# Performance work log

Hardware: AMD Instinct MI355X
Metric: run time of the kernel (lower is better)

Reference implementation:

```python
import jax, jax.numpy as jnp
import numpy as np

D_MODEL = 1024
NUM_HEADS = 16
D_K = D_MODEL // NUM_HEADS
ROPE_BASE = 10000.0


def _rotate_half(x):
    # interleaved pairs: (x0, x1) -> (-x1, x0)
    x1 = x[..., ::2]
    x2 = x[..., 1::2]
    return jnp.stack((-x2, x1), axis=-1).reshape(x.shape)


def _rope(q, k):
    seq_len = q.shape[-2]
    freqs = ROPE_BASE ** (jnp.arange(0, D_K, 2, dtype=q.dtype) / D_K)  # [D_K/2]
    angles = jnp.arange(seq_len, dtype=q.dtype)[:, None] / freqs[None, :]  # [S, D_K/2]
    sin = jnp.repeat(jnp.sin(angles), 2, axis=-1)[None, None]  # [1,1,S,D_K]
    cos = jnp.repeat(jnp.cos(angles), 2, axis=-1)[None, None]
    return q * cos + _rotate_half(q) * sin, k * cos + _rotate_half(k) * sin


def setup_inputs() -> dict:
    key = jax.random.key(0)
    ks = jax.random.split(key, 9)
    B, S, D = 2, 2048, D_MODEL
    s = 1.0 / np.sqrt(D)
    inp = {
        "x": jax.random.normal(ks[0], (B, S, D), dtype=jnp.float32),
        "wq": jax.random.uniform(ks[1], (D, D), jnp.float32, -s, s),
        "bq": jax.random.uniform(ks[2], (D,), jnp.float32, -s, s),
        "wk": jax.random.uniform(ks[3], (D, D), jnp.float32, -s, s),
        "bk": jax.random.uniform(ks[4], (D,), jnp.float32, -s, s),
        "wv": jax.random.uniform(ks[5], (D, D), jnp.float32, -s, s),
        "bv": jax.random.uniform(ks[6], (D,), jnp.float32, -s, s),
        "wo": jax.random.uniform(ks[7], (D, D), jnp.float32, -s, s),
        "bo": jax.random.uniform(ks[8], (D,), jnp.float32, -s, s),
    }
    return inp


def reference(x, wq, bq, wk, bk, wv, bv, wo, bo):
    B, S, D = x.shape
    H, dk = NUM_HEADS, D_K
    # torch Linear: y = x @ W.T + b
    Q = (x @ wq.T + bq).reshape(B, S, H, dk).transpose(0, 2, 1, 3)  # [B,H,S,dk]
    K = (x @ wk.T + bk).reshape(B, S, H, dk).transpose(0, 2, 1, 3)
    V = (x @ wv.T + bv).reshape(B, S, H, dk).transpose(0, 2, 1, 3)
    Q, K = _rope(Q, K)
    score = jnp.einsum("bhqd,bhkd->bhqk", Q, K) / jnp.sqrt(jnp.asarray(dk, x.dtype))
    attn_w = jax.nn.softmax(score, axis=-1)
    out = jnp.einsum("bhqk,bhkd->bhqd", attn_w, V)  # [B,H,S,dk]
    out = out.transpose(0, 2, 1, 3).reshape(B, S, D)
    return out @ wo.T + bo
```

## Files before the change

### kernel.cpp

```cpp
#include <hip/hip_runtime.h>
#include <hip/hip_bf16.h>
#include <math.h>

typedef __bf16 bf16_t;
typedef __bf16 bf16x4_t __attribute__((ext_vector_type(4)));
typedef __bf16 bf16x8_t __attribute__((ext_vector_type(8)));
typedef float  f32x4_t  __attribute__((ext_vector_type(4)));

#define SEQ 2048
#define DM  1024
#define NH  16
#define DK  64
#define ROPE_C 0.4152410118609203f
#define EXP_C (1.4426950408889634f / 8.0f)

#define GLD16(gp, lp) \
  __builtin_amdgcn_global_load_lds((__attribute__((address_space(1))) const void*)(gp), \
                                   (__attribute__((address_space(3))) void*)(lp), 16, 0, 0)

__global__ __launch_bounds__(256)
void prep_kernel(const float* __restrict__ x,  const float* __restrict__ wq,
                 const float* __restrict__ wk, const float* __restrict__ wv,
                 const float* __restrict__ wo, bf16_t* __restrict__ dst,
                 float2* __restrict__ lut) {
  if (blockIdx.x < 8192) {
    int i = blockIdx.x * 256 + threadIdx.x;
    const float* s;
    if (i < 1048576) {
      s = x + (size_t)i * 4;
    } else {
      int j = i - 1048576;
      int w = j >> 18;
      const float* base = (w == 0) ? wq : (w == 1) ? wk : (w == 2) ? wv : wo;
      s = base + (size_t)(j & 262143) * 4;
    }
    float4 v = *(const float4*)s;
    bf16x4_t o;
    o.x = (bf16_t)v.x; o.y = (bf16_t)v.y; o.z = (bf16_t)v.z; o.w = (bf16_t)v.w;
    ((bf16x4_t*)dst)[i] = o;
  } else {
    int i = (blockIdx.x - 8192) * 256 + threadIdx.x;
    int s = i >> 5, f = i & 31;
    float ang = (float)s * exp2f(-ROPE_C * (float)f);
    float sn, cs;
    sincosf(ang, &sn, &cs);
    lut[i] = make_float2(sn, cs);
  }
}

__global__ __launch_bounds__(256, 3)
void gemm_qkv(const bf16_t* __restrict__ A, const bf16_t* __restrict__ Wq,
              const bf16_t* __restrict__ Wk, const bf16_t* __restrict__ Wv,
              const float* __restrict__ bq, const float* __restrict__ bk,
              const float* __restrict__ bv, const float2* __restrict__ lut,
              bf16_t* __restrict__ Qb, bf16_t* __restrict__ Kb,
              bf16_t* __restrict__ Vtb) {
  const int K = 1024;
  __shared__ bf16_t As[128 * 64];
  __shared__ bf16_t Bs[128 * 64];

  const int tid  = threadIdx.x;
  const int w    = tid >> 6;
  const int lane = tid & 63;
  const int quad = lane >> 4;
  const int lrow = lane & 15;
  const int wm = (w >> 1) * 64, wn = (w & 1) * 64;

  const int srow8 = lane >> 3;
  const int scolz = (((lane & 7) ^ (lane >> 3)) * 8);

  const int id   = blockIdx.x;
  const int xcd  = id & 7;
  const int rank = id >> 3;
  const int isV  = rank >= 64;

  const bf16_t* Ablk;
  const bf16_t* Bblk;
  int bmQK = 0, bnl = 0, isK = 0, bmF = 0, bnT = 0;
  if (!isV) {
    const int q = xcd * 64 + rank;
    bmQK = q >> 4;
    const int bn = q & 15;
    isK = bn >> 3;
    bnl = bn & 7;
    Ablk = A + (size_t)(bmQK * 128) * K;
    Bblk = (isK ? Wk : Wq) + (size_t)(bnl * 128) * K;
  } else {
    const int v = xcd * 32 + (rank - 64);
    bnT = v >> 3;
    bmF = v & 7;
    Ablk = Wv + (size_t)(bmF * 128) * K;
    Bblk = A + (size_t)(bnT * 128) * K;
  }

  f32x4_t acc[4][4] = {};

  for (int k0 = 0; k0 < K; k0 += 64) {
#pragma unroll
    for (int i = 0; i < 4; i++) {
      GLD16(&Ablk[(size_t)(w * 32 + i * 8 + srow8) * K + k0 + scolz], &As[(w * 32 + i * 8) * 64]);
      GLD16(&Bblk[(size_t)(w * 32 + i * 8 + srow8) * K + k0 + scolz], &Bs[(w * 32 + i * 8) * 64]);
    }
    __syncthreads();

#pragma unroll
    for (int kk = 0; kk < 2; kk++) {
      const int gsw = (((kk << 2) | quad) ^ (lrow & 7)) * 8;
      bf16x8_t af[4], bf[4];
#pragma unroll
      for (int mi = 0; mi < 4; mi++)
        af[mi] = *(const bf16x8_t*)(&As[(wm + mi * 16 + lrow) * 64 + gsw]);
#pragma unroll
      for (int ni = 0; ni < 4; ni++)
        bf[ni] = *(const bf16x8_t*)(&Bs[(wn + ni * 16 + lrow) * 64 + gsw]);
#pragma unroll
      for (int mi = 0; mi < 4; mi++)
#pragma unroll
        for (int ni = 0; ni < 4; ni++)
          acc[mi][ni] = __builtin_amdgcn_mfma_f32_16x16x32_bf16(af[mi], bf[ni], acc[mi][ni], 0, 0, 0);
    }
    __syncthreads();
  }

  if (!isV) {
    const int brow = bmQK * 128 + wm;
    const int cbase = bnl * 128 + wn;
    const float* bias = isK ? bk : bq;
    bf16_t* D = isK ? Kb : Qb;

#pragma unroll
    for (int ni = 0; ni < 4; ni++) {
      const int col = cbase + ni * 16 + lrow;
      const float bvv = bias[col];
      const int t = col & 63;
      const int h = col >> 6;
      const int fidx = t >> 1;
#pragma unroll
      for (int mi = 0; mi < 4; mi++) {
        f32x4_t v = acc[mi][ni];
#pragma unroll
        for (int r = 0; r < 4; r++) {
          const int row = brow + mi * 16 + quad * 4 + r;
          const int s = row & (SEQ - 1);
          float val = v[r] + bvv;
          const float2 sc = lut[s * 32 + fidx];
          const float pv = __shfl_xor(val, 1);
          val = (t & 1) ? (val * sc.y + pv * sc.x) : (val * sc.y - pv * sc.x);
          const int b = row >> 11;
          const size_t o = (((size_t)(b * NH + h) * SEQ) + s) * DK + t;
          D[o] = (bf16_t)val;
        }
      }
    }
  } else {
    const int fbase = bmF * 128 + wm;
    const int tbase = bnT * 128 + wn;

#pragma unroll
    for (int ni = 0; ni < 4; ni++) {
      const int t = tbase + ni * 16 + lrow;
      const int b = t >> 11;
      const int s = t & (SEQ - 1);
#pragma unroll
      for (int mi = 0; mi < 4; mi++) {
        f32x4_t v = acc[mi][ni];
        const int f = fbase + mi * 16 + quad * 4;
        const int h = f >> 6, d = f & 63;
#pragma unroll
        for (int r = 0; r < 4; r++)
          Vtb[((size_t)((b * NH + h) * DK + d + r)) * SEQ + s] = (bf16_t)(v[r] + bv[f + r]);
      }
    }
  }
}

__global__ __launch_bounds__(256)
void gemm_out(const bf16_t* __restrict__ A, const bf16_t* __restrict__ Bw,
              const float* __restrict__ bias, float* __restrict__ D) {
  const int K = 1024;
  __shared__ bf16_t As[128 * 64];
  __shared__ bf16_t Bs[64 * 64];

  const int tid  = threadIdx.x;
  const int w    = tid >> 6;
  const int lane = tid & 63;
  const int quad = lane >> 4;
  const int lrow = lane & 15;
  const int wm = (w >> 1) * 64, wn = (w & 1) * 32;

  const int srow8 = lane >> 3;
  const int scolz = (((lane & 7) ^ (lane >> 3)) * 8);

  const int id  = blockIdx.x;
  const int swz = (id & 7) * 64 + (id >> 3);
  const int bm  = swz >> 4;
  const int bn  = swz & 15;

  const bf16_t* Ablk = A  + (size_t)(bm * 128) * K;
  const bf16_t* Bblk = Bw + (size_t)(bn * 64) * K;

  f32x4_t acc[4][2] = {};

  for (int k0 = 0; k0 < K; k0 += 64) {
#pragma unroll
    for (int i = 0; i < 4; i++)
      GLD16(&Ablk[(size_t)(w * 32 + i * 8 + srow8) * K + k0 + scolz], &As[(w * 32 + i * 8) * 64]);
#pragma unroll
    for (int i = 0; i < 2; i++)
      GLD16(&Bblk[(size_t)(w * 16 + i * 8 + srow8) * K + k0 + scolz], &Bs[(w * 16 + i * 8) * 64]);
    __syncthreads();

#pragma unroll
    for (int kk = 0; kk < 2; kk++) {
      const int gsw = (((kk << 2) | quad) ^ (lrow & 7)) * 8;
      bf16x8_t af[4], bf[2];
#pragma unroll
      for (int mi = 0; mi < 4; mi++)
        af[mi] = *(const bf16x8_t*)(&As[(wm + mi * 16 + lrow) * 64 + gsw]);
#pragma unroll
      for (int ni = 0; ni < 2; ni++)
        bf[ni] = *(const bf16x8_t*)(&Bs[(wn + ni * 16 + lrow) * 64 + gsw]);
#pragma unroll
      for (int mi = 0; mi < 4; mi++)
#pragma unroll
        for (int ni = 0; ni < 2; ni++)
          acc[mi][ni] = __builtin_amdgcn_mfma_f32_16x16x32_bf16(af[mi], bf[ni], acc[mi][ni], 0, 0, 0);
    }
    __syncthreads();
  }

#pragma unroll
  for (int ni = 0; ni < 2; ni++) {
    const int col = bn * 64 + wn + ni * 16 + lrow;
    const float bvv = bias[col];
#pragma unroll
    for (int mi = 0; mi < 4; mi++) {
      f32x4_t v = acc[mi][ni];
#pragma unroll
      for (int r = 0; r < 4; r++) {
        const int row = bm * 128 + wm + mi * 16 + quad * 4 + r;
        D[(size_t)row * DM + col] = v[r] + bvv;
      }
    }
  }
}

__global__ __launch_bounds__(512)
void attn_kernel(const bf16_t* __restrict__ Q, const bf16_t* __restrict__ K,
                 const bf16_t* __restrict__ Vt, bf16_t* __restrict__ AO) {
  __shared__ bf16_t Ks[2][128 * 64];
  __shared__ bf16_t Vs[2][64 * 128];

  const int tid  = threadIdx.x;
  const int w    = tid >> 6;
  const int lane = tid & 63;
  const int quad = lane >> 4;
  const int lrow = lane & 15;

  const int id  = blockIdx.x;
  const int swz = (id & 7) * 64 + (id >> 3);
  const int bh  = swz >> 4;
  const int q0  = (swz & 15) * 128 + w * 16;

  const bf16_t* Qh  = Q  + (size_t)bh * SEQ * DK;
  const bf16_t* Kh  = K  + (size_t)bh * SEQ * DK;
  const bf16_t* Vth = Vt + (size_t)bh * DK * SEQ;

  bf16x8_t qf[2];
#pragma unroll
  for (int c = 0; c < 2; c++) {
    bf16x8_t t = *(const bf16x8_t*)(&Qh[(size_t)(q0 + lrow) * DK + c * 32 + quad * 8]);
#pragma unroll
    for (int i = 0; i < 8; i++) t[i] = (bf16_t)((float)t[i] * EXP_C);
    qf[c] = t;
  }

  f32x4_t accO[4] = {};
  float lsum = 0.f;

  const int krow = tid >> 2;
  const int kcol = (tid & 3) * 16;
  const int kg0  = (tid & 3) * 2;
  const int vrow = tid >> 3;
  const int vcol = (tid & 7) * 16;

  const int kw0 = krow * 64 + ((kg0       ^ (krow & 7)) << 3);
  const int kw1 = krow * 64 + (((kg0 + 1) ^ (krow & 7)) << 3);
  const int vb  = (vcol >> 5) * 4;
  const int vh  = ((vcol >> 4) & 1) * 4;
  const int vsw = vrow & 15;
  const int vw0 = vrow * 128 + (((vb + 0) ^ vsw) << 3) + vh;
  const int vw1 = vrow * 128 + (((vb + 1) ^ vsw) << 3) + vh;
  const int vw2 = vrow * 128 + (((vb + 2) ^ vsw) << 3) + vh;
  const int vw3 = vrow * 128 + (((vb + 3) ^ vsw) << 3) + vh;

  uint4 kr0 = *(const uint4*)(&Kh[(size_t)krow * DK + kcol]);
  uint4 kr1 = *(const uint4*)(&Kh[(size_t)krow * DK + kcol + 8]);
  uint4 vr0 = *(const uint4*)(&Vth[(size_t)vrow * SEQ + vcol]);
  uint4 vr1 = *(const uint4*)(&Vth[(size_t)vrow * SEQ + vcol + 8]);
  *(uint4*)(&Ks[0][kw0]) = kr0;
  *(uint4*)(&Ks[0][kw1]) = kr1;
  *(uint2*)(&Vs[0][vw0]) = make_uint2(vr0.x, vr0.y);
  *(uint2*)(&Vs[0][vw1]) = make_uint2(vr0.z, vr0.w);
  *(uint2*)(&Vs[0][vw2]) = make_uint2(vr1.x, vr1.y);
  *(uint2*)(&Vs[0][vw3]) = make_uint2(vr1.z, vr1.w);
  __syncthreads();

#pragma unroll 2
  for (int kt = 0; kt < SEQ / 128; ++kt) {
    const int cur = kt & 1, nxt = cur ^ 1;
    const bool more = (kt + 1 < SEQ / 128);

    if (more) {
      const int kb = (kt + 1) * 128;
      kr0 = *(const uint4*)(&Kh[(size_t)(kb + krow) * DK + kcol]);
      kr1 = *(const uint4*)(&Kh[(size_t)(kb + krow) * DK + kcol + 8]);
      vr0 = *(const uint4*)(&Vth[(size_t)vrow * SEQ + kb + vcol]);
      vr1 = *(const uint4*)(&Vth[(size_t)vrow * SEQ + kb + vcol + 8]);
    }

    __builtin_amdgcn_s_setprio(1);
#pragma unroll
    for (int c2 = 0; c2 < 4; ++c2) {
      uint2 pk[2];
#pragma unroll
      for (int kk2 = 0; kk2 < 2; ++kk2) {
        const int kk = c2 * 2 + kk2;
        const int krd = (kk * 16 + lrow) * 64;
        bf16x8_t kf0 = *(const bf16x8_t*)(&Ks[cur][krd + ((quad       ^ (lrow & 7)) << 3)]);
        bf16x8_t kf1 = *(const bf16x8_t*)(&Ks[cur][krd + (((quad + 4) ^ (lrow & 7)) << 3)]);
        f32x4_t z = {};
        z = __builtin_amdgcn_mfma_f32_16x16x32_bf16(kf0, qf[0], z, 0, 0, 0);
        z = __builtin_amdgcn_mfma_f32_16x16x32_bf16(kf1, qf[1], z, 0, 0, 0);
        const float p0 = __builtin_amdgcn_exp2f(z[0]), p1 = __builtin_amdgcn_exp2f(z[1]);
        const float p2 = __builtin_amdgcn_exp2f(z[2]), p3 = __builtin_amdgcn_exp2f(z[3]);
        lsum += (p0 + p1) + (p2 + p3);
        pk[kk2].x = __builtin_amdgcn_perm(__builtin_bit_cast(unsigned, p1),
                                          __builtin_bit_cast(unsigned, p0), 0x07060302u);
        pk[kk2].y = __builtin_amdgcn_perm(__builtin_bit_cast(unsigned, p3),
                                          __builtin_bit_cast(unsigned, p2), 0x07060302u);
      }
      uint4 pfu;
      pfu.x = pk[0].x; pfu.y = pk[0].y; pfu.z = pk[1].x; pfu.w = pk[1].y;
      bf16x8_t pf = __builtin_bit_cast(bf16x8_t, pfu);
#pragma unroll
      for (int nt = 0; nt < 4; ++nt) {
        bf16x8_t vf = *(const bf16x8_t*)(
            &Vs[cur][(nt * 16 + lrow) * 128 + ((((c2 << 2) | quad) ^ lrow) << 3)]);
        accO[nt] = __builtin_amdgcn_mfma_f32_16x16x32_bf16(pf, vf, accO[nt], 0, 0, 0);
      }
    }
    __builtin_amdgcn_s_setprio(0);

    if (more) {
      *(uint4*)(&Ks[nxt][kw0]) = kr0;
      *(uint4*)(&Ks[nxt][kw1]) = kr1;
      *(uint2*)(&Vs[nxt][vw0]) = make_uint2(vr0.x, vr0.y);
      *(uint2*)(&Vs[nxt][vw1]) = make_uint2(vr0.z, vr0.w);
      *(uint2*)(&Vs[nxt][vw2]) = make_uint2(vr1.x, vr1.y);
      *(uint2*)(&Vs[nxt][vw3]) = make_uint2(vr1.z, vr1.w);
    }
    __syncthreads();
  }

  lsum += __shfl_xor(lsum, 16);
  lsum += __shfl_xor(lsum, 32);
  float linv[4];
#pragma unroll
  for (int r = 0; r < 4; r++)
    linv[r] = 1.0f / __shfl(lsum, quad * 4 + r);

  const int b = bh >> 4, h = bh & 15;
#pragma unroll
  for (int nt = 0; nt < 4; nt++)
#pragma unroll
    for (int r = 0; r < 4; r++) {
      const int srowq = q0 + quad * 4 + r;
      const float val = accO[nt][r] * linv[r];
      const size_t o = ((size_t)(b * SEQ + srowq)) * DM + h * DK + nt * 16 + lrow;
      AO[o] = (bf16_t)val;
    }
}

extern "C" void kernel_launch(void* const* d_in, const int* in_sizes, int n_in,
                              void* d_out, int out_size, void* d_ws, size_t ws_size,
                              hipStream_t stream) {
  const float* x  = (const float*)d_in[0];
  const float* wq = (const float*)d_in[1];
  const float* bq = (const float*)d_in[2];
  const float* wk = (const float*)d_in[3];
  const float* bk = (const float*)d_in[4];
  const float* wv = (const float*)d_in[5];
  const float* bv = (const float*)d_in[6];
  const float* wo = (const float*)d_in[7];
  const float* bo = (const float*)d_in[8];
  float* out = (float*)d_out;

  char* ws = (char*)d_ws;
  bf16_t* xb   = (bf16_t*)(ws);
  bf16_t* wqb  = (bf16_t*)(ws + 8388608);
  bf16_t* wkb  = (bf16_t*)(ws + 10485760);
  bf16_t* wvb  = (bf16_t*)(ws + 12582912);
  bf16_t* wob  = (bf16_t*)(ws + 14680064);
  bf16_t* Qb   = (bf16_t*)(ws + 16777216);
  bf16_t* Kb   = (bf16_t*)(ws + 25165824);
  bf16_t* Vtb  = (bf16_t*)(ws + 33554432);
  bf16_t* AOb  = (bf16_t*)(ws + 41943040);
  float2* lut  = (float2*)(ws + 50331648);

  prep_kernel<<<8448, 256, 0, stream>>>(x, wq, wk, wv, wo, xb, lut);

  gemm_qkv<<<768, 256, 0, stream>>>(xb, wqb, wkb, wvb, bq, bk, bv, lut, Qb, Kb, Vtb);

  attn_kernel<<<512, 512, 0, stream>>>(Qb, Kb, Vtb, AOb);

  gemm_out<<<512, 256, 0, stream>>>(AOb, wob, bo, out);
}
```

Baseline: 184.8 us.

## Split KV sequence across two thread groups per attention block and merge via LDS

Doubles the attention block to 1024 threads; each 512-thread half processes half of the key/value sequence with its own single LDS buffer and register prefetch. Partial row sums and output accumulators are combined through shared memory at the end before normalization and the bf16 store. This is meant to increase waves in flight and shorten the per-block serial KV loop. In exchange it loses LDS double buffering, adds a final reduction, and the launch bound may pressure registers.

```diff
diff --git a/kernel.cpp b/kernel.cpp
--- a/kernel.cpp
+++ b/kernel.cpp
@@ -245,14 +245,19 @@
   }
 }
 
-__global__ __launch_bounds__(512)
+__global__ __launch_bounds__(1024, 8)
 void attn_kernel(const bf16_t* __restrict__ Q, const bf16_t* __restrict__ K,
                  const bf16_t* __restrict__ Vt, bf16_t* __restrict__ AO) {
-  __shared__ bf16_t Ks[2][128 * 64];
-  __shared__ bf16_t Vs[2][64 * 128];
+  __shared__ __align__(16) char smem[66560];
+  bf16_t* Ks  = (bf16_t*)smem;
+  bf16_t* Vsm = (bf16_t*)(smem + 32768);
+  float*  Lx  = (float*)(smem + 65536);
+  float*  Ox  = (float*)smem;
 
   const int tid  = threadIdx.x;
-  const int w    = tid >> 6;
+  const int grp  = tid >> 9;
+  const int t5   = tid & 511;
+  const int w    = (tid >> 6) & 7;
   const int lane = tid & 63;
   const int quad = lane >> 4;
   const int lrow = lane & 15;
@@ -265,6 +270,7 @@
   const bf16_t* Qh  = Q  + (size_t)bh * SEQ * DK;
   const bf16_t* Kh  = K  + (size_t)bh * SEQ * DK;
   const bf16_t* Vth = Vt + (size_t)bh * DK * SEQ;
+  const int kofs = grp * 1024;
 
   bf16x8_t qf[2];
 #pragma unroll
@@ -278,41 +284,39 @@
   f32x4_t accO[4] = {};
   float lsum = 0.f;
 
-  const int krow = tid >> 2;
-  const int kcol = (tid & 3) * 16;
-  const int kg0  = (tid & 3) * 2;
-  const int vrow = tid >> 3;
-  const int vcol = (tid & 7) * 16;
-
-  const int kw0 = krow * 64 + ((kg0       ^ (krow & 7)) << 3);
-  const int kw1 = krow * 64 + (((kg0 + 1) ^ (krow & 7)) << 3);
+  const int krow = t5 >> 2;
+  const int kcol = (t5 & 3) * 16;
+  const int kg0  = (t5 & 3) * 2;
+  const int vrow = t5 >> 3;
+  const int vcol = (t5 & 7) * 16;
+
+  const int kbase = grp * 8192;
+  const int kw0 = kbase + krow * 64 + ((kg0       ^ (krow & 7)) << 3);
+  const int kw1 = kbase + krow * 64 + (((kg0 + 1) ^ (krow & 7)) << 3);
   const int vb  = (vcol >> 5) * 4;
   const int vh  = ((vcol >> 4) & 1) * 4;
   const int vsw = vrow & 15;
-  const int vw0 = vrow * 128 + (((vb + 0) ^ vsw) << 3) + vh;
-  const int vw1 = vrow * 128 + (((vb + 1) ^ vsw) << 3) + vh;
-  const int vw2 = vrow * 128 + (((vb + 2) ^ vsw) << 3) + vh;
-  const int vw3 = vrow * 128 + (((vb + 3) ^ vsw) << 3) + vh;
-
-  uint4 kr0 = *(const uint4*)(&Kh[(size_t)krow * DK + kcol]);
-  uint4 kr1 = *(const uint4*)(&Kh[(size_t)krow * DK + kcol + 8]);
-  uint4 vr0 = *(const uint4*)(&Vth[(size_t)vrow * SEQ + vcol]);
-  uint4 vr1 = *(const uint4*)(&Vth[(size_t)vrow * SEQ + vcol + 8]);
-  *(uint4*)(&Ks[0][kw0]) = kr0;
-  *(uint4*)(&Ks[0][kw1]) = kr1;
-  *(uint2*)(&Vs[0][vw0]) = make_uint2(vr0.x, vr0.y);
-  *(uint2*)(&Vs[0][vw1]) = make_uint2(vr0.z, vr0.w);
-  *(uint2*)(&Vs[0][vw2]) = make_uint2(vr1.x, vr1.y);
-  *(uint2*)(&Vs[0][vw3]) = make_uint2(vr1.z, vr1.w);
-  __syncthreads();
-
-#pragma unroll 2
-  for (int kt = 0; kt < SEQ / 128; ++kt) {
-    const int cur = kt & 1, nxt = cur ^ 1;
-    const bool more = (kt + 1 < SEQ / 128);
-
-    if (more) {
-      const int kb = (kt + 1) * 128;
+  const int vw0 = kbase + vrow * 128 + (((vb + 0) ^ vsw) << 3) + vh;
+  const int vw1 = kbase + vrow * 128 + (((vb + 1) ^ vsw) << 3) + vh;
+  const int vw2 = kbase + vrow * 128 + (((vb + 2) ^ vsw) << 3) + vh;
+  const int vw3 = kbase + vrow * 128 + (((vb + 3) ^ vsw) << 3) + vh;
+
+  uint4 kr0 = *(const uint4*)(&Kh[(size_t)(kofs + krow) * DK + kcol]);
+  uint4 kr1 = *(const uint4*)(&Kh[(size_t)(kofs + krow) * DK + kcol + 8]);
+  uint4 vr0 = *(const uint4*)(&Vth[(size_t)vrow * SEQ + kofs + vcol]);
+  uint4 vr1 = *(const uint4*)(&Vth[(size_t)vrow * SEQ + kofs + vcol + 8]);
+
+  for (int kt = 0; kt < 8; ++kt) {
+    *(uint4*)(&Ks[kw0])  = kr0;
+    *(uint4*)(&Ks[kw1])  = kr1;
+    *(uint2*)(&Vsm[vw0]) = make_uint2(vr0.x, vr0.y);
+    *(uint2*)(&Vsm[vw1]) = make_uint2(vr0.z, vr0.w);
+    *(uint2*)(&Vsm[vw2]) = make_uint2(vr1.x, vr1.y);
+    *(uint2*)(&Vsm[vw3]) = make_uint2(vr1.z, vr1.w);
+    __syncthreads();
+
+    if (kt + 1 < 8) {
+      const int kb = kofs + (kt + 1) * 128;
       kr0 = *(const uint4*)(&Kh[(size_t)(kb + krow) * DK + kcol]);
       kr1 = *(const uint4*)(&Kh[(size_t)(kb + krow) * DK + kcol + 8]);
       vr0 = *(const uint4*)(&Vth[(size_t)vrow * SEQ + kb + vcol]);
@@ -326,9 +330,9 @@
 #pragma unroll
       for (int kk2 = 0; kk2 < 2; ++kk2) {
         const int kk = c2 * 2 + kk2;
-        const int krd = (kk * 16 + lrow) * 64;
-        bf16x8_t kf0 = *(const bf16x8_t*)(&Ks[cur][krd + ((quad       ^ (lrow & 7)) << 3)]);
-        bf16x8_t kf1 = *(const bf16x8_t*)(&Ks[cur][krd + (((quad + 4) ^ (lrow & 7)) << 3)]);
+        const int krd = kbase + (kk * 16 + lrow) * 64;
+        bf16x8_t kf0 = *(const bf16x8_t*)(&Ks[krd + ((quad       ^ (lrow & 7)) << 3)]);
+        bf16x8_t kf1 = *(const bf16x8_t*)(&Ks[krd + (((quad + 4) ^ (lrow & 7)) << 3)]);
         f32x4_t z = {};
         z = __builtin_amdgcn_mfma_f32_16x16x32_bf16(kf0, qf[0], z, 0, 0, 0);
         z = __builtin_amdgcn_mfma_f32_16x16x32_bf16(kf1, qf[1], z, 0, 0, 0);
@@ -346,40 +350,42 @@
 #pragma unroll
       for (int nt = 0; nt < 4; ++nt) {
         bf16x8_t vf = *(const bf16x8_t*)(
-            &Vs[cur][(nt * 16 + lrow) * 128 + ((((c2 << 2) | quad) ^ lrow) << 3)]);
+            &Vsm[kbase + (nt * 16 + lrow) * 128 + ((((c2 << 2) | quad) ^ lrow) << 3)]);
         accO[nt] = __builtin_amdgcn_mfma_f32_16x16x32_bf16(pf, vf, accO[nt], 0, 0, 0);
       }
     }
     __builtin_amdgcn_s_setprio(0);
-
-    if (more) {
-      *(uint4*)(&Ks[nxt][kw0]) = kr0;
-      *(uint4*)(&Ks[nxt][kw1]) = kr1;
-      *(uint2*)(&Vs[nxt][vw0]) = make_uint2(vr0.x, vr0.y);
-      *(uint2*)(&Vs[nxt][vw1]) = make_uint2(vr0.z, vr0.w);
-      *(uint2*)(&Vs[nxt][vw2]) = make_uint2(vr1.x, vr1.y);
-      *(uint2*)(&Vs[nxt][vw3]) = make_uint2(vr1.z, vr1.w);
-    }
     __syncthreads();
   }
 
   lsum += __shfl_xor(lsum, 16);
   lsum += __shfl_xor(lsum, 32);
-  float linv[4];
-#pragma unroll
-  for (int r = 0; r < 4; r++)
-    linv[r] = 1.0f / __shfl(lsum, quad * 4 + r);
-
-  const int b = bh >> 4, h = bh & 15;
-#pragma unroll
-  for (int nt = 0; nt < 4; nt++)
+  if (quad == 0) Lx[grp * 128 + w * 16 + lrow] = lsum;
+
+  if (grp == 1) {
+#pragma unroll
+    for (int nt = 0; nt < 4; nt++)
+#pragma unroll
+      for (int r = 0; r < 4; r++)
+        Ox[(w * 16 + quad * 4 + r) * 68 + nt * 16 + lrow] = accO[nt][r];
+  }
+  __syncthreads();
+
+  if (grp == 0) {
+    const int b = bh >> 4, h = bh & 15;
 #pragma unroll
     for (int r = 0; r < 4; r++) {
+      const int rl = w * 16 + quad * 4 + r;
+      const float linv = 1.0f / (Lx[rl] + Lx[128 + rl]);
       const int srowq = q0 + quad * 4 + r;
-      const float val = accO[nt][r] * linv[r];
-      const size_t o = ((size_t)(b * SEQ + srowq)) * DM + h * DK + nt * 16 + lrow;
-      AO[o] = (bf16_t)val;
-    }
+#pragma unroll
+      for (int nt = 0; nt < 4; nt++) {
+        const float val = (accO[nt][r] + Ox[rl * 68 + nt * 16 + lrow]) * linv;
+        const size_t o = ((size_t)(b * SEQ + srowq)) * DM + h * DK + nt * 16 + lrow;
+        AO[o] = (bf16_t)val;
+      }
+    }
+  }
 }
 
 extern "C" void kernel_launch(void* const* d_in, const int* in_sizes, int n_in,
@@ -412,7 +418,7 @@
 
   gemm_qkv<<<768, 256, 0, stream>>>(xb, wqb, wkb, wvb, bq, bk, bv, lut, Qb, Kb, Vtb);
 
-  attn_kernel<<<512, 512, 0, stream>>>(Qb, Kb, Vtb, AOb);
+  attn_kernel<<<512, 1024, 0, stream>>>(Qb, Kb, Vtb, AOb);
 
   gemm_out<<<512, 256, 0, stream>>>(AOb, wob, bo, out);
 }
```

After: 238.6 us. +29.1%, slower.
